# Kernel tuning notes

Hardware: AMD Instinct MI355X
Metric: run time of the kernel (lower is better)

The kernel has to match this reference:

```python
import jax, jax.numpy as jnp
import numpy as np

B, C, H, W = 8, 192, 128, 128
FILTERS = (1, 3, 3, 3, 3, 1)
BOUND = 1e-9


def setup_inputs() -> dict:
    key = jax.random.key(0)
    ks = jax.random.split(key, 16)
    d = {"x": jax.random.normal(ks[0], (B, C, H, W), jnp.float32)}
    for i in range(5):
        d[f"m{i}"] = jax.random.normal(ks[1 + i], (C, FILTERS[i + 1], FILTERS[i]), jnp.float32) * 0.5
        d[f"b{i}"] = jax.random.uniform(ks[6 + i], (C, FILTERS[i + 1], 1), jnp.float32, -0.5, 0.5)
    for i in range(4):
        d[f"f{i}"] = jax.random.normal(ks[11 + i], (C, FILTERS[i + 1], 1), jnp.float32) * 0.1
    return d


def _logits_cumulative(x, ms, bs, fs):
    # x: (C, 1, N); per-channel tiny MLP: matmul(softplus(M), x) + b, tanh gate
    logits = x
    for i in range(5):
        logits = jnp.matmul(jax.nn.softplus(ms[i]), logits) + bs[i]
        if i < 4:
            logits = logits + jnp.tanh(fs[i]) * jnp.tanh(logits)
    return logits


def reference(x, m0, m1, m2, m3, m4, b0, b1, b2, b3, b4, f0, f1, f2, f3):
    ms = (m0, m1, m2, m3, m4)
    bs = (b0, b1, b2, b3, b4)
    fs = (f0, f1, f2, f3)
    # quantize: per-sample min/max over (C,H,W), round to 16-bit grid
    x_min = jnp.min(x, axis=(1, 2, 3), keepdims=True)
    x_max = jnp.max(x, axis=(1, 2, 3), keepdims=True)
    xq = jnp.round((x - x_min) * 65535.0 / (x_max - x_min + 1e-12))
    xd = xq / 65535.0  # dequantize
    # permute (B,C,H,W)->(C,B,H,W), reshape to (C,1,N)
    xp = jnp.transpose(xd, (1, 0, 2, 3)).reshape(C, 1, -1)
    lower = _logits_cumulative(xp - 0.5, ms, bs, fs)
    upper = _logits_cumulative(xp + 0.5, ms, bs, fs)
    likelihood = jax.nn.sigmoid(upper) - jax.nn.sigmoid(lower)
    likelihood = jnp.maximum(likelihood, BOUND)  # LowerBound forward
    x_out = jnp.transpose(xp.reshape(C, B, H, W), (1, 0, 2, 3))
    likelihood = jnp.transpose(likelihood.reshape(C, B, H, W), (1, 0, 2, 3))
    return (x_out, likelihood)
```

## Files before the change

### kernel.cpp

```cpp
#include <hip/hip_runtime.h>
#include <math.h>

#define CCH 192
#define BATCH 8
#define HWSZ 16384
#define NPER (CCH * HWSZ)
#define NTOT ((size_t)BATCH * NPER)
#define INV65535 (1.0f / 65535.0f)

#define TABN    8193
#define TABSTR  8196
#define TSCALE  (8192.0f / 65535.0f)

#define WS_WTAB_OFF_FLOATS 64
#define WS_TAB_OFF_BYTES   65536
#define WS_NEEDED (WS_TAB_OFF_BYTES + (size_t)CCH * TABSTR * 4)

#define RED_BLOCKS_PER_SAMPLE 192
#define MINMAX_BLOCKS (BATCH * RED_BLOCKS_PER_SAMPLE)
#define TAB_BLOCKS (CCH * 33)

typedef float f4 __attribute__((ext_vector_type(4)));

__device__ __forceinline__ unsigned f2u_ord(float f) {
    unsigned u = __float_as_uint(f);
    return (u & 0x80000000u) ? ~u : (u | 0x80000000u);
}
__device__ __forceinline__ float u2f_ord(unsigned u) {
    return __uint_as_float((u & 0x80000000u) ? (u ^ 0x80000000u) : ~u);
}
__device__ __forceinline__ float fexp2(float x) { return __builtin_amdgcn_exp2f(x); }
__device__ __forceinline__ float frcp(float x)  { return __builtin_amdgcn_rcpf(x); }
__device__ __forceinline__ float ftanh(float x) {
    return 1.0f - 2.0f * frcp(fexp2(2.8853900817779268f * x) + 1.0f);
}
__device__ __forceinline__ float fsig(float x) {
    return frcp(1.0f + fexp2(-1.4426950408889634f * x));
}

__device__ __forceinline__ float eval_mlp(float x, const float* W)
{
    float a0 = fmaf(W[0], x, W[33]);
    float a1 = fmaf(W[1], x, W[34]);
    float a2 = fmaf(W[2], x, W[35]);
    a0 = fmaf(W[46], ftanh(a0), a0);
    a1 = fmaf(W[47], ftanh(a1), a1);
    a2 = fmaf(W[48], ftanh(a2), a2);

    float c0 = fmaf(W[3], a0, fmaf(W[4],  a1, fmaf(W[5],  a2, W[36])));
    float c1 = fmaf(W[6], a0, fmaf(W[7],  a1, fmaf(W[8],  a2, W[37])));
    float c2 = fmaf(W[9], a0, fmaf(W[10], a1, fmaf(W[11], a2, W[38])));
    c0 = fmaf(W[49], ftanh(c0), c0);
    c1 = fmaf(W[50], ftanh(c1), c1);
    c2 = fmaf(W[51], ftanh(c2), c2);

    float d0 = fmaf(W[12], c0, fmaf(W[13], c1, fmaf(W[14], c2, W[39])));
    float d1 = fmaf(W[15], c0, fmaf(W[16], c1, fmaf(W[17], c2, W[40])));
    float d2 = fmaf(W[18], c0, fmaf(W[19], c1, fmaf(W[20], c2, W[41])));
    d0 = fmaf(W[52], ftanh(d0), d0);
    d1 = fmaf(W[53], ftanh(d1), d1);
    d2 = fmaf(W[54], ftanh(d2), d2);

    float e0 = fmaf(W[21], d0, fmaf(W[22], d1, fmaf(W[23], d2, W[42])));
    float e1 = fmaf(W[24], d0, fmaf(W[25], d1, fmaf(W[26], d2, W[43])));
    float e2 = fmaf(W[27], d0, fmaf(W[28], d1, fmaf(W[29], d2, W[44])));
    e0 = fmaf(W[55], ftanh(e0), e0);
    e1 = fmaf(W[56], ftanh(e1), e1);
    e2 = fmaf(W[57], ftanh(e2), e2);

    return fmaf(W[30], e0, fmaf(W[31], e1, fmaf(W[32], e2, W[45])));
}

__device__ __forceinline__ float eval_lik(float d, const float* W)
{
    float lo = eval_mlp(d - 0.5f, W);
    float up = eval_mlp(d + 0.5f, W);
    return fmaxf(fsig(up) - fsig(lo), 1e-9f);
}

__device__ __forceinline__ void minmax_block(const float* __restrict__ x,
                                             unsigned* __restrict__ mm,
                                             int bid)
{
    int b   = bid / RED_BLOCKS_PER_SAMPLE;
    int blk = bid % RED_BLOCKS_PER_SAMPLE;
    const f4* xs = (const f4*)(x + (size_t)b * NPER);
    int base = blk * 4096;
    float mn = INFINITY, mx = -INFINITY;
    #pragma unroll
    for (int i = 0; i < 16; ++i) {
        f4 v = xs[base + i * 256 + threadIdx.x];
        mn = fminf(mn, fminf(fminf(v.x, v.y), fminf(v.z, v.w)));
        mx = fmaxf(mx, fmaxf(fmaxf(v.x, v.y), fmaxf(v.z, v.w)));
    }
    #pragma unroll
    for (int off = 32; off > 0; off >>= 1) {
        mn = fminf(mn, __shfl_down(mn, off, 64));
        mx = fmaxf(mx, __shfl_down(mx, off, 64));
    }
    __shared__ float smn[4], smx[4];
    int wave = threadIdx.x >> 6;
    if ((threadIdx.x & 63) == 0) { smn[wave] = mn; smx[wave] = mx; }
    __syncthreads();
    if (threadIdx.x == 0) {
        #pragma unroll
        for (int i = 1; i < 4; ++i) { mn = fminf(mn, smn[i]); mx = fmaxf(mx, smx[i]); }
        atomicMin(&mm[b],     f2u_ord(mn));
        atomicMin(&mm[8 + b], ~f2u_ord(mx));
    }
}

__global__ __launch_bounds__(256) void prep_kernel(
    const float* __restrict__ x, unsigned* __restrict__ mm,
    const float* __restrict__ m0, const float* __restrict__ b0,
    const float* __restrict__ m1, const float* __restrict__ b1,
    const float* __restrict__ m2, const float* __restrict__ b2,
    const float* __restrict__ m3, const float* __restrict__ b3,
    const float* __restrict__ m4, const float* __restrict__ b4,
    const float* __restrict__ f0, const float* __restrict__ f1,
    const float* __restrict__ f2, const float* __restrict__ f3,
    float* __restrict__ tab)
{
    if (blockIdx.x < MINMAX_BLOCKS) {
        minmax_block(x, mm, blockIdx.x);
        return;
    }
    int tb = blockIdx.x - MINMAX_BLOCKS;
    int c  = tb / 33;
    int jc = tb % 33;
    int t  = threadIdx.x;

    __shared__ float sW[58];
    if (t < 58) {
        float v;
        if (t < 33) {
            if      (t < 3)  v = m0[c * 3 + t];
            else if (t < 12) v = m1[c * 9 + t - 3];
            else if (t < 21) v = m2[c * 9 + t - 12];
            else if (t < 30) v = m3[c * 9 + t - 21];
            else             v = m4[c * 3 + t - 30];
            v = fmaxf(v, 0.f) + log1pf(expf(-fabsf(v)));
        } else if (t < 46) {
            int i = t - 33;
            if      (i < 3)  v = b0[c * 3 + i];
            else if (i < 6)  v = b1[c * 3 + i - 3];
            else if (i < 9)  v = b2[c * 3 + i - 6];
            else if (i < 12) v = b3[c * 3 + i - 9];
            else             v = b4[c];
        } else {
            int i = t - 46;
            if      (i < 3)  v = f0[c * 3 + i];
            else if (i < 6)  v = f1[c * 3 + i - 3];
            else if (i < 9)  v = f2[c * 3 + i - 6];
            else             v = f3[c * 3 + i - 9];
            v = tanhf(v);
        }
        sW[t] = v;
    }
    __syncthreads();

    float W[58];
    #pragma unroll
    for (int i = 0; i < 58; ++i) W[i] = sW[i];

    int j = jc * 256 + t;
    if (j < TABN) {
        float d = (float)j * (1.0f / 8192.0f);
        tab[(size_t)c * TABSTR + j] = eval_lik(d, W);
    }
}

__global__ __launch_bounds__(256) void gather_kernel(const float* __restrict__ x,
                                                     const unsigned* __restrict__ mm,
                                                     const float* __restrict__ tab,
                                                     float* __restrict__ out)
{
    __shared__ __align__(16) float ltab[TABN + 3];

    int c = blockIdx.x >> 3;
    int b = blockIdx.x & 7;
    int t = threadIdx.x;

    const f4* tsrc = (const f4*)(tab + (size_t)c * TABSTR);
    f4* tdst = (f4*)ltab;
    #pragma unroll
    for (int i = 0; i < 8; ++i) tdst[i * 256 + t] = tsrc[i * 256 + t];
    if (t == 0) ltab[8192] = tab[(size_t)c * TABSTR + 8192];
    __syncthreads();

    float mn = u2f_ord(mm[b]);
    float mx = u2f_ord(~mm[8 + b]);
    float scale = 65535.0f / (mx - mn + 1e-12f);

    size_t base = ((size_t)b * CCH + c) * HWSZ;
    const f4* xin = (const f4*)(x + base);
    f4* o0 = (f4*)(out + base);
    f4* o1 = (f4*)(out + NTOT + base);

    auto proc = [&](float xi, float& od, float& ol) {
        float kf   = rintf((xi - mn) * scale);
        od         = kf * INV65535;
        float tpos = kf * TSCALE;
        int   j    = (int)tpos;
        j = j > 8191 ? 8191 : j;
        float frac = tpos - (float)j;
        float t0 = ltab[j];
        float t1 = ltab[j + 1];
        ol = fmaxf(fmaf(frac, t1 - t0, t0), 1e-9f);
    };

    #pragma unroll
    for (int i = 0; i < 16; ++i) {
        f4 v = __builtin_nontemporal_load(&xin[i * 256 + t]);
        float in[4] = {v.x, v.y, v.z, v.w};
        float xd[4], lk[4];
        #pragma unroll
        for (int k = 0; k < 4; ++k) proc(in[k], xd[k], lk[k]);
        f4 vxd = {xd[0], xd[1], xd[2], xd[3]};
        f4 vlk = {lk[0], lk[1], lk[2], lk[3]};
        __builtin_nontemporal_store(vxd, &o0[i * 256 + t]);
        __builtin_nontemporal_store(vlk, &o1[i * 256 + t]);
    }
}

__global__ void setup_kernel(const float* __restrict__ m0, const float* __restrict__ b0,
                             const float* __restrict__ m1, const float* __restrict__ b1,
                             const float* __restrict__ m2, const float* __restrict__ b2,
                             const float* __restrict__ m3, const float* __restrict__ b3,
                             const float* __restrict__ m4, const float* __restrict__ b4,
                             const float* __restrict__ f0, const float* __restrict__ f1,
                             const float* __restrict__ f2, const float* __restrict__ f3,
                             float* __restrict__ wtab)
{
    int t = threadIdx.x;
    if (t < CCH) {
        float* w = wtab + t * 64;
        #pragma unroll
        for (int i = 0; i < 3; ++i) { float v = m0[t*3+i]; w[i]    = fmaxf(v,0.f)+log1pf(expf(-fabsf(v))); }
        #pragma unroll
        for (int i = 0; i < 9; ++i) { float v = m1[t*9+i]; w[3+i]  = fmaxf(v,0.f)+log1pf(expf(-fabsf(v))); }
        #pragma unroll
        for (int i = 0; i < 9; ++i) { float v = m2[t*9+i]; w[12+i] = fmaxf(v,0.f)+log1pf(expf(-fabsf(v))); }
        #pragma unroll
        for (int i = 0; i < 9; ++i) { float v = m3[t*9+i]; w[21+i] = fmaxf(v,0.f)+log1pf(expf(-fabsf(v))); }
        #pragma unroll
        for (int i = 0; i < 3; ++i) { float v = m4[t*3+i]; w[30+i] = fmaxf(v,0.f)+log1pf(expf(-fabsf(v))); }
        #pragma unroll
        for (int i = 0; i < 3; ++i) w[33+i] = b0[t*3+i];
        #pragma unroll
        for (int i = 0; i < 3; ++i) w[36+i] = b1[t*3+i];
        #pragma unroll
        for (int i = 0; i < 3; ++i) w[39+i] = b2[t*3+i];
        #pragma unroll
        for (int i = 0; i < 3; ++i) w[42+i] = b3[t*3+i];
        w[45] = b4[t];
        #pragma unroll
        for (int i = 0; i < 3; ++i) w[46+i] = tanhf(f0[t*3+i]);
        #pragma unroll
        for (int i = 0; i < 3; ++i) w[49+i] = tanhf(f1[t*3+i]);
        #pragma unroll
        for (int i = 0; i < 3; ++i) w[52+i] = tanhf(f2[t*3+i]);
        #pragma unroll
        for (int i = 0; i < 3; ++i) w[55+i] = tanhf(f3[t*3+i]);
    }
}

__global__ __launch_bounds__(256) void ebott_main(const float* __restrict__ x,
                                                  const unsigned* __restrict__ mm,
                                                  const float* __restrict__ wtab,
                                                  float* __restrict__ out)
{
    int blk = blockIdx.x;
    int q   = blk & 3;
    int c   = (blk >> 2) % CCH;
    int b   = blk / (4 * CCH);

    float W[58];
    const float* w = wtab + c * 64;
    #pragma unroll
    for (int i = 0; i < 58; ++i) W[i] = w[i];

    float mn = u2f_ord(mm[b]);
    float mx = u2f_ord(~mm[8 + b]);
    float scale = 65535.0f / (mx - mn + 1e-12f);

    size_t base = (size_t)(b * CCH + c) * HWSZ + q * 4096;
    const f4* xin = (const f4*)(x + base);
    f4* o0 = (f4*)(out + base);
    f4* o1 = (f4*)(out + NTOT + base);
    int t = threadIdx.x;

    #pragma unroll
    for (int i = 0; i < 4; ++i) {
        f4 v = xin[i * 256 + t];
        float in[4] = {v.x, v.y, v.z, v.w};
        float xd[4], lk[4];
        #pragma unroll
        for (int k = 0; k < 4; ++k) {
            float d = rintf((in[k] - mn) * scale) * INV65535;
            xd[k] = d;
            lk[k] = eval_lik(d, W);
        }
        f4 vxd = {xd[0], xd[1], xd[2], xd[3]};
        f4 vlk = {lk[0], lk[1], lk[2], lk[3]};
        o0[i * 256 + t] = vxd;
        o1[i * 256 + t] = vlk;
    }
}

extern "C" void kernel_launch(void* const* d_in, const int* in_sizes, int n_in,
                              void* d_out, int out_size, void* d_ws, size_t ws_size,
                              hipStream_t stream)
{
    const float* x  = (const float*)d_in[0];
    const float* m0 = (const float*)d_in[1];
    const float* b0 = (const float*)d_in[2];
    const float* m1 = (const float*)d_in[3];
    const float* b1 = (const float*)d_in[4];
    const float* m2 = (const float*)d_in[5];
    const float* b2 = (const float*)d_in[6];
    const float* m3 = (const float*)d_in[7];
    const float* b3 = (const float*)d_in[8];
    const float* m4 = (const float*)d_in[9];
    const float* b4 = (const float*)d_in[10];
    const float* f0 = (const float*)d_in[11];
    const float* f1 = (const float*)d_in[12];
    const float* f2 = (const float*)d_in[13];
    const float* f3 = (const float*)d_in[14];

    unsigned* mm = (unsigned*)d_ws;
    float* wtab  = (float*)d_ws + WS_WTAB_OFF_FLOATS;
    float* tab   = (float*)((char*)d_ws + WS_TAB_OFF_BYTES);
    float* out   = (float*)d_out;

    hipMemsetAsync(d_ws, 0xFF, 64, stream);

    if (ws_size >= WS_NEEDED) {
        prep_kernel<<<MINMAX_BLOCKS + TAB_BLOCKS, 256, 0, stream>>>(
            x, mm, m0, b0, m1, b1, m2, b2, m3, b3, m4, b4, f0, f1, f2, f3, tab);
        gather_kernel<<<CCH * BATCH, 256, 0, stream>>>(x, mm, tab, out);
    } else {
        setup_kernel<<<1, 256, 0, stream>>>(m0, b0, m1, b1, m2, b2, m3, b3, m4, b4,
                                            f0, f1, f2, f3, wtab);
        prep_kernel<<<MINMAX_BLOCKS, 256, 0, stream>>>(
            x, mm, m0, b0, m1, b1, m2, b2, m3, b3, m4, b4, f0, f1, f2, f3, tab);
        ebott_main<<<BATCH * CCH * 4, 256, 0, stream>>>(x, mm, wtab, out);
    }
}
```

Measured before the change: 337.4 us.

## Replace atomic min/max with partials and reuse LDS table across two batches

The global atomic min/max and its memset are replaced by per-block partial min/max arrays, which the gather kernel reduces itself. Each gather block now handles two batch planes for one channel, so the per-channel lookup table is loaded into LDS half as often, and the first input vector is prefetched before the table copy. The cost is half as many blocks (768), which means less parallelism and more serial work per block. Each block also does an extra small reduction over 192 partials for each of its two samples.

```diff
diff --git a/kernel.cpp b/kernel.cpp
--- a/kernel.cpp
+++ b/kernel.cpp
@@ -12,7 +12,9 @@
 #define TABSTR  8196
 #define TSCALE  (8192.0f / 65535.0f)
 
-#define WS_WTAB_OFF_FLOATS 64
+#define WS_PMN_OFF_FLOATS  64
+#define WS_PMX_OFF_FLOATS  2048
+#define WS_WTAB_OFF_FLOATS 4096
 #define WS_TAB_OFF_BYTES   65536
 #define WS_NEEDED (WS_TAB_OFF_BYTES + (size_t)CCH * TABSTR * 4)
 
@@ -22,13 +24,6 @@
 
 typedef float f4 __attribute__((ext_vector_type(4)));
 
-__device__ __forceinline__ unsigned f2u_ord(float f) {
-    unsigned u = __float_as_uint(f);
-    return (u & 0x80000000u) ? ~u : (u | 0x80000000u);
-}
-__device__ __forceinline__ float u2f_ord(unsigned u) {
-    return __uint_as_float((u & 0x80000000u) ? (u ^ 0x80000000u) : ~u);
-}
 __device__ __forceinline__ float fexp2(float x) { return __builtin_amdgcn_exp2f(x); }
 __device__ __forceinline__ float frcp(float x)  { return __builtin_amdgcn_rcpf(x); }
 __device__ __forceinline__ float ftanh(float x) {
@@ -79,7 +74,8 @@
 }
 
 __device__ __forceinline__ void minmax_block(const float* __restrict__ x,
-                                             unsigned* __restrict__ mm,
+                                             float* __restrict__ pmn,
+                                             float* __restrict__ pmx,
                                              int bid)
 {
     int b   = bid / RED_BLOCKS_PER_SAMPLE;
@@ -105,13 +101,14 @@
     if (threadIdx.x == 0) {
         #pragma unroll
         for (int i = 1; i < 4; ++i) { mn = fminf(mn, smn[i]); mx = fmaxf(mx, smx[i]); }
-        atomicMin(&mm[b],     f2u_ord(mn));
-        atomicMin(&mm[8 + b], ~f2u_ord(mx));
+        pmn[bid] = mn;
+        pmx[bid] = mx;
     }
 }
 
 __global__ __launch_bounds__(256) void prep_kernel(
-    const float* __restrict__ x, unsigned* __restrict__ mm,
+    const float* __restrict__ x,
+    float* __restrict__ pmn, float* __restrict__ pmx,
     const float* __restrict__ m0, const float* __restrict__ b0,
     const float* __restrict__ m1, const float* __restrict__ b1,
     const float* __restrict__ m2, const float* __restrict__ b2,
@@ -122,7 +119,7 @@
     float* __restrict__ tab)
 {
     if (blockIdx.x < MINMAX_BLOCKS) {
-        minmax_block(x, mm, blockIdx.x);
+        minmax_block(x, pmn, pmx, blockIdx.x);
         return;
     }
     int tb = blockIdx.x - MINMAX_BLOCKS;
@@ -171,33 +168,60 @@
 }
 
 __global__ __launch_bounds__(256) void gather_kernel(const float* __restrict__ x,
-                                                     const unsigned* __restrict__ mm,
+                                                     const float* __restrict__ pmn,
+                                                     const float* __restrict__ pmx,
                                                      const float* __restrict__ tab,
                                                      float* __restrict__ out)
 {
     __shared__ __align__(16) float ltab[TABN + 3];
-
-    int c = blockIdx.x >> 3;
-    int b = blockIdx.x & 7;
-    int t = threadIdx.x;
+    __shared__ float red[4][4];
+
+    int c  = blockIdx.x >> 2;
+    int p  = blockIdx.x & 3;
+    int b0 = p;
+    int b1 = p + 4;
+    int t  = threadIdx.x;
+
+    size_t base0 = ((size_t)b0 * CCH + c) * HWSZ;
+    size_t base1 = ((size_t)b1 * CCH + c) * HWSZ;
+    const f4* xin0 = (const f4*)(x + base0);
+    const f4* xin1 = (const f4*)(x + base1);
+
+    f4 pf0 = __builtin_nontemporal_load(&xin0[t]);
+    f4 pf1 = __builtin_nontemporal_load(&xin1[t]);
 
     const f4* tsrc = (const f4*)(tab + (size_t)c * TABSTR);
     f4* tdst = (f4*)ltab;
     #pragma unroll
     for (int i = 0; i < 8; ++i) tdst[i * 256 + t] = tsrc[i * 256 + t];
     if (t == 0) ltab[8192] = tab[(size_t)c * TABSTR + 8192];
+
+    float mn0 = t < 192 ? pmn[b0 * RED_BLOCKS_PER_SAMPLE + t] :  INFINITY;
+    float mx0 = t < 192 ? pmx[b0 * RED_BLOCKS_PER_SAMPLE + t] : -INFINITY;
+    float mn1 = t < 192 ? pmn[b1 * RED_BLOCKS_PER_SAMPLE + t] :  INFINITY;
+    float mx1 = t < 192 ? pmx[b1 * RED_BLOCKS_PER_SAMPLE + t] : -INFINITY;
+    #pragma unroll
+    for (int off = 32; off > 0; off >>= 1) {
+        mn0 = fminf(mn0, __shfl_down(mn0, off, 64));
+        mx0 = fmaxf(mx0, __shfl_down(mx0, off, 64));
+        mn1 = fminf(mn1, __shfl_down(mn1, off, 64));
+        mx1 = fmaxf(mx1, __shfl_down(mx1, off, 64));
+    }
+    int wave = t >> 6;
+    if ((t & 63) == 0) {
+        red[wave][0] = mn0; red[wave][1] = mx0;
+        red[wave][2] = mn1; red[wave][3] = mx1;
+    }
     __syncthreads();
 
-    float mn = u2f_ord(mm[b]);
-    float mx = u2f_ord(~mm[8 + b]);
-    float scale = 65535.0f / (mx - mn + 1e-12f);
-
-    size_t base = ((size_t)b * CCH + c) * HWSZ;
-    const f4* xin = (const f4*)(x + base);
-    f4* o0 = (f4*)(out + base);
-    f4* o1 = (f4*)(out + NTOT + base);
-
-    auto proc = [&](float xi, float& od, float& ol) {
+    mn0 = fminf(fminf(red[0][0], red[1][0]), fminf(red[2][0], red[3][0]));
+    mx0 = fmaxf(fmaxf(red[0][1], red[1][1]), fmaxf(red[2][1], red[3][1]));
+    mn1 = fminf(fminf(red[0][2], red[1][2]), fminf(red[2][2], red[3][2]));
+    mx1 = fmaxf(fmaxf(red[0][3], red[1][3]), fmaxf(red[2][3], red[3][3]));
+    float scale0 = 65535.0f / (mx0 - mn0 + 1e-12f);
+    float scale1 = 65535.0f / (mx1 - mn1 + 1e-12f);
+
+    auto proc = [&](float xi, float mn, float scale, float& od, float& ol) {
         float kf   = rintf((xi - mn) * scale);
         od         = kf * INV65535;
         float tpos = kf * TSCALE;
@@ -209,18 +233,23 @@
         ol = fmaxf(fmaf(frac, t1 - t0, t0), 1e-9f);
     };
 
-    #pragma unroll
-    for (int i = 0; i < 16; ++i) {
-        f4 v = __builtin_nontemporal_load(&xin[i * 256 + t]);
-        float in[4] = {v.x, v.y, v.z, v.w};
-        float xd[4], lk[4];
-        #pragma unroll
-        for (int k = 0; k < 4; ++k) proc(in[k], xd[k], lk[k]);
-        f4 vxd = {xd[0], xd[1], xd[2], xd[3]};
-        f4 vlk = {lk[0], lk[1], lk[2], lk[3]};
-        __builtin_nontemporal_store(vxd, &o0[i * 256 + t]);
-        __builtin_nontemporal_store(vlk, &o1[i * 256 + t]);
-    }
+    auto plane = [&](const f4* xin, f4* o0, f4* o1, float mn, float scale, f4 pf) {
+        #pragma unroll
+        for (int i = 0; i < 16; ++i) {
+            f4 v = (i == 0) ? pf : __builtin_nontemporal_load(&xin[i * 256 + t]);
+            float in[4] = {v.x, v.y, v.z, v.w};
+            float xd[4], lk[4];
+            #pragma unroll
+            for (int k = 0; k < 4; ++k) proc(in[k], mn, scale, xd[k], lk[k]);
+            f4 vxd = {xd[0], xd[1], xd[2], xd[3]};
+            f4 vlk = {lk[0], lk[1], lk[2], lk[3]};
+            __builtin_nontemporal_store(vxd, &o0[i * 256 + t]);
+            __builtin_nontemporal_store(vlk, &o1[i * 256 + t]);
+        }
+    };
+
+    plane(xin0, (f4*)(out + base0), (f4*)(out + NTOT + base0), mn0, scale0, pf0);
+    plane(xin1, (f4*)(out + base1), (f4*)(out + NTOT + base1), mn1, scale1, pf1);
 }
 
 __global__ void setup_kernel(const float* __restrict__ m0, const float* __restrict__ b0,
@@ -266,7 +295,8 @@
 }
 
 __global__ __launch_bounds__(256) void ebott_main(const float* __restrict__ x,
-                                                  const unsigned* __restrict__ mm,
+                                                  const float* __restrict__ pmn,
+                                                  const float* __restrict__ pmx,
                                                   const float* __restrict__ wtab,
                                                   float* __restrict__ out)
 {
@@ -280,8 +310,11 @@
     #pragma unroll
     for (int i = 0; i < 58; ++i) W[i] = w[i];
 
-    float mn = u2f_ord(mm[b]);
-    float mx = u2f_ord(~mm[8 + b]);
+    float mn = INFINITY, mx = -INFINITY;
+    for (int i = 0; i < RED_BLOCKS_PER_SAMPLE; ++i) {
+        mn = fminf(mn, pmn[b * RED_BLOCKS_PER_SAMPLE + i]);
+        mx = fmaxf(mx, pmx[b * RED_BLOCKS_PER_SAMPLE + i]);
+    }
     float scale = 65535.0f / (mx - mn + 1e-12f);
 
     size_t base = (size_t)(b * CCH + c) * HWSZ + q * 4096;
@@ -328,22 +361,21 @@
     const float* f2 = (const float*)d_in[13];
     const float* f3 = (const float*)d_in[14];
 
-    unsigned* mm = (unsigned*)d_ws;
-    float* wtab  = (float*)d_ws + WS_WTAB_OFF_FLOATS;
-    float* tab   = (float*)((char*)d_ws + WS_TAB_OFF_BYTES);
-    float* out   = (float*)d_out;
-
-    hipMemsetAsync(d_ws, 0xFF, 64, stream);
+    float* pmn  = (float*)d_ws + WS_PMN_OFF_FLOATS;
+    float* pmx  = (float*)d_ws + WS_PMX_OFF_FLOATS;
+    float* wtab = (float*)d_ws + WS_WTAB_OFF_FLOATS;
+    float* tab  = (float*)((char*)d_ws + WS_TAB_OFF_BYTES);
+    float* out  = (float*)d_out;
 
     if (ws_size >= WS_NEEDED) {
         prep_kernel<<<MINMAX_BLOCKS + TAB_BLOCKS, 256, 0, stream>>>(
-            x, mm, m0, b0, m1, b1, m2, b2, m3, b3, m4, b4, f0, f1, f2, f3, tab);
-        gather_kernel<<<CCH * BATCH, 256, 0, stream>>>(x, mm, tab, out);
+            x, pmn, pmx, m0, b0, m1, b1, m2, b2, m3, b3, m4, b4, f0, f1, f2, f3, tab);
+        gather_kernel<<<CCH * 4, 256, 0, stream>>>(x, pmn, pmx, tab, out);
     } else {
         setup_kernel<<<1, 256, 0, stream>>>(m0, b0, m1, b1, m2, b2, m3, b3, m4, b4,
                                             f0, f1, f2, f3, wtab);
         prep_kernel<<<MINMAX_BLOCKS, 256, 0, stream>>>(
-            x, mm, m0, b0, m1, b1, m2, b2, m3, b3, m4, b4, f0, f1, f2, f3, tab);
-        ebott_main<<<BATCH * CCH * 4, 256, 0, stream>>>(x, mm, wtab, out);
-    }
-}
+            x, pmn, pmx, m0, b0, m1, b1, m2, b2, m3, b3, m4, b4, f0, f1, f2, f3, tab);
+        ebott_main<<<BATCH * CCH * 4, 256, 0, stream>>>(x, pmn, pmx, wtab, out);
+    }
+}
```

Measured after the change: 324.3 us. 1.04x faster.
